# Kernel optimization log

Hardware: AMD Instinct MI355X
Metric: run time of the kernel (lower is better)

## Reference

```python
import jax, jax.numpy as jnp
import numpy as np

H = 16      # query heads
KV = 4      # kv heads
HD = 128    # head dim
THETA = 10000.0
NEG = -1e9


def _rope_tables(S, dtype):
    inv_freq = 1.0 / (THETA ** (jnp.arange(0, HD, 2, dtype=jnp.float32) / HD))
    ang = jnp.arange(S, dtype=jnp.float32)[:, None] * inv_freq[None, :]  # [S, HD/2]
    emb = jnp.concatenate([ang, ang], axis=-1)  # [S, HD]
    return jnp.cos(emb).astype(dtype), jnp.sin(emb).astype(dtype)


def _rotate_half(x):
    x1, x2 = jnp.split(x, 2, axis=-1)
    return jnp.concatenate([-x2, x1], axis=-1)


def _apply_rope(t, cos, sin):
    # t: [B, h, S, HD]; cos/sin: [S, HD]
    return t * cos[None, None] + _rotate_half(t) * sin[None, None]


def setup_inputs() -> dict:
    key = jax.random.key(0)
    ks = jax.random.split(key, 5)
    B, S, D = 2, 2048, 2048
    sc = 0.02
    return {
        "x": jax.random.normal(ks[0], (B, S, D), jnp.float32),
        "wq": jax.random.normal(ks[1], (D, D), jnp.float32) * sc,
        "wk": jax.random.normal(ks[2], (KV * HD, D), jnp.float32) * sc,
        "wv": jax.random.normal(ks[3], (KV * HD, D), jnp.float32) * sc,
        "wo": jax.random.normal(ks[4], (D, D), jnp.float32) * sc,
    }


def reference(x, wq, wk, wv, wo):
    B, S, D = x.shape
    q = (x @ wq.T).reshape(B, S, H, HD).transpose(0, 2, 1, 3)   # [B,H,S,HD]
    k = (x @ wk.T).reshape(B, S, KV, HD).transpose(0, 2, 1, 3)  # [B,KV,S,HD]
    v = (x @ wv.T).reshape(B, S, KV, HD).transpose(0, 2, 1, 3)

    cos, sin = _rope_tables(S, x.dtype)
    q = _apply_rope(q, cos, sin)
    k = _apply_rope(k, cos, sin)

    # GQA: repeat kv heads to match query heads (q_group_num = H // KV)
    k = jnp.repeat(k, H // KV, axis=1)  # [B,H,S,HD]
    v = jnp.repeat(v, H // KV, axis=1)

    scores = jnp.einsum("bhqd,bhkd->bhqk", q, k) / jnp.sqrt(jnp.float32(HD)).astype(x.dtype)
    causal = jnp.where(jnp.tril(jnp.ones((S, S), bool)), 0.0, NEG).astype(jnp.float32)
    attn = jax.nn.softmax(scores.astype(jnp.float32) + causal, axis=-1).astype(x.dtype)

    out = jnp.einsum("bhqk,bhkd->bhqd", attn, v)  # [B,H,S,HD]
    out = out.transpose(0, 2, 1, 3).reshape(B, S, D)
    return out @ wo.T
```

## Files before the change

### kernel.cpp

```cpp
#include <hip/hip_runtime.h>
#include <math.h>

typedef unsigned short u16;
typedef __attribute__((ext_vector_type(8))) short short8;
typedef __attribute__((ext_vector_type(8))) __bf16 bf16x8;
typedef __attribute__((ext_vector_type(4))) float floatx4;
typedef __attribute__((ext_vector_type(16))) float floatx16;
typedef __attribute__((ext_vector_type(4))) unsigned short u16x4;
typedef __attribute__((ext_vector_type(4))) float float4v;
typedef __attribute__((ext_vector_type(4))) unsigned int uint4v;

static __device__ __forceinline__ float b2f(u16 u) {
  unsigned int x = ((unsigned int)u) << 16;
  return __builtin_bit_cast(float, x);
}
static __device__ __forceinline__ u16 f2b(float f) {
  unsigned int x = __builtin_bit_cast(unsigned int, f);
  x += 0x7fffu + ((x >> 16) & 1u);
  return (u16)(x >> 16);
}
static __device__ __forceinline__ unsigned int pk2(float lo, float hi) {
  unsigned int r;
  asm("v_cvt_pk_bf16_f32 %0, %1, %2" : "=v"(r) : "v"(lo), "v"(hi));
  return r;
}
static __device__ __forceinline__ void gload_lds16(const void* g, void* l) {
  __builtin_amdgcn_global_load_lds(
      (const __attribute__((address_space(1))) unsigned int*)g,
      (__attribute__((address_space(3))) unsigned int*)l, 16, 0, 0);
}

__global__ __launch_bounds__(256) void cvt5_kernel(
    const float* __restrict__ x, const float* __restrict__ wq,
    const float* __restrict__ wk, const float* __restrict__ wv,
    const float* __restrict__ wo, u16* __restrict__ xb, u16* __restrict__ wqb,
    u16* __restrict__ wkb, u16* __restrict__ wvb, u16* __restrict__ wob) {
  int bid = blockIdx.x;
  const float* in;
  u16* out;
  int i0;
  if (bid < 8192) { in = x; out = xb; i0 = bid; }
  else if (bid < 12288) { in = wq; out = wqb; i0 = bid - 8192; }
  else if (bid < 13312) { in = wk; out = wkb; i0 = bid - 12288; }
  else if (bid < 14336) { in = wv; out = wvb; i0 = bid - 13312; }
  else { in = wo; out = wob; i0 = bid - 14336; }
  int i = i0 * 256 + threadIdx.x;
  float4v v = reinterpret_cast<const float4v*>(in)[i];
  u16x4 o;
  o[0] = f2b(v[0]); o[1] = f2b(v[1]); o[2] = f2b(v[2]); o[3] = f2b(v[3]);
  reinterpret_cast<u16x4*>(out)[i] = o;
}

__global__ __launch_bounds__(256) void rope_table_kernel(float* __restrict__ ct,
                                                         float* __restrict__ st) {
  int idx = blockIdx.x * 256 + threadIdx.x;
  int s = idx >> 6, j = idx & 63;
  float inv = powf(10000.0f, -(float)j * (1.0f / 64.0f));
  float ang = (float)s * inv;
  ct[idx] = cosf(ang);
  st[idx] = sinf(ang);
}

__global__ __launch_bounds__(256) void rope_k_kernel(const u16* __restrict__ in,
                                                     u16* __restrict__ out,
                                                     const float* __restrict__ ct,
                                                     const float* __restrict__ st) {
  int idx = blockIdx.x * 256 + threadIdx.x;
  int jc = idx & 7;
  int rest = idx >> 3;
  int h = rest & 3;
  int bs = rest >> 2;
  int s = bs & 2047;
  int b = bs >> 11;
  int j0 = jc * 8;
  size_t inoff = (size_t)bs * 3072 + 2048 + h * 128 + j0;
  short8 lo = *reinterpret_cast<const short8*>(&in[inoff]);
  short8 hi = *reinterpret_cast<const short8*>(&in[inoff + 64]);
  short8 o0, o1;
#pragma unroll
  for (int e = 0; e < 8; ++e) {
    float c = ct[s * 64 + j0 + e], sn = st[s * 64 + j0 + e];
    float t1 = b2f((u16)lo[e]);
    float t2 = b2f((u16)hi[e]);
    o0[e] = (short)f2b(t1 * c - t2 * sn);
    o1[e] = (short)f2b(t2 * c + t1 * sn);
  }
  size_t ooff = ((size_t)(b * 4 + h) * 2048 + s) * 128 + j0;
  *reinterpret_cast<short8*>(&out[ooff]) = o0;
  *reinterpret_cast<short8*>(&out[ooff + 64]) = o1;
}

__global__ __launch_bounds__(256) void vtrans_kernel(const u16* __restrict__ in,
                                                     u16* __restrict__ out) {
  __shared__ u16 t[128][66];
  int s0 = blockIdx.x * 64;
  int b = blockIdx.y >> 2, kv = blockIdx.y & 3;
  int tid = threadIdx.x;
#pragma unroll
  for (int it = 0; it < 32; ++it) {
    int idx = it * 256 + tid;
    int sl = idx >> 7, d = idx & 127;
    t[d][sl] = in[(size_t)(b * 2048 + s0 + sl) * 3072 + 2560 + kv * 128 + d];
  }
  __syncthreads();
#pragma unroll
  for (int it = 0; it < 32; ++it) {
    int idx = it * 256 + tid;
    int d = idx >> 6, sl = idx & 63;
    out[(size_t)((b * 4 + kv) * 128 + d) * 2048 + s0 + sl] = t[d][sl];
  }
}

static __device__ __forceinline__ void store_out(u16* p, float v) { *p = f2b(v); }
static __device__ __forceinline__ void store_out(float* p, float v) { *p = v; }

template <typename OutT>
__global__ __launch_bounds__(256) void gemm_bt(const u16* __restrict__ A,
                                               const u16* __restrict__ B,
                                               OutT* __restrict__ C, int M, int N, int K) {
  __shared__ __align__(16) u16 Al[128 * 32];
  __shared__ __align__(16) u16 Bl[128 * 32];
  const int tid = threadIdx.x;
  const int lane = tid & 63;
  const int w = tid >> 6;
  const int wr = w >> 1, wc = w & 1;
  const int lr = lane & 15, lg = lane >> 4;
  const int brow = blockIdx.y, bcol = blockIdx.x;
  const int r0 = lane >> 2, kp = lane & 3;
  const u16* Ag = A + (size_t)(brow * 128) * K;
  const u16* Bg = B + (size_t)(bcol * 128) * K;
  floatx4 acc[4][4] = {};
  for (int k0 = 0; k0 < K; k0 += 32) {
#pragma unroll
    for (int j = 0; j < 2; ++j) {
      int c = w * 2 + j;
      int row = c * 16 + r0;
      gload_lds16(Ag + (size_t)row * K + k0 + kp * 8, &Al[c * 512]);
      gload_lds16(Bg + (size_t)row * K + k0 + kp * 8, &Bl[c * 512]);
    }
    __syncthreads();
    bf16x8 af[4], bfr[4];
#pragma unroll
    for (int m = 0; m < 4; ++m)
      af[m] = *reinterpret_cast<const bf16x8*>(&Al[(wr * 64 + m * 16 + lr) * 32 + lg * 8]);
#pragma unroll
    for (int n = 0; n < 4; ++n)
      bfr[n] = *reinterpret_cast<const bf16x8*>(&Bl[(wc * 64 + n * 16 + lr) * 32 + lg * 8]);
#pragma unroll
    for (int m = 0; m < 4; ++m)
#pragma unroll
      for (int n = 0; n < 4; ++n)
        acc[m][n] = __builtin_amdgcn_mfma_f32_16x16x32_bf16(af[m], bfr[n], acc[m][n], 0, 0, 0);
    __syncthreads();
  }
#pragma unroll
  for (int m = 0; m < 4; ++m) {
    int row = brow * 128 + wr * 64 + m * 16 + lg * 4;
#pragma unroll
    for (int n = 0; n < 4; ++n) {
      int col = bcol * 128 + wc * 64 + n * 16 + lr;
#pragma unroll
      for (int i = 0; i < 4; ++i) store_out(&C[(size_t)(row + i) * N + col], acc[m][n][i]);
    }
  }
}

__global__ __launch_bounds__(256, 2) void attn_kernel(const u16* __restrict__ QKV,
                                                      const u16* __restrict__ K,
                                                      const u16* __restrict__ V,
                                                      const float* __restrict__ ct,
                                                      const float* __restrict__ st,
                                                      u16* __restrict__ O) {
  __shared__ __align__(16) u16 Kl[2][64 * 128];
  __shared__ __align__(16) u16 Vl[2][128 * 64];
  const int tid = threadIdx.x, lane = tid & 63, w = tid >> 6;
  const int ql = lane & 31, h2 = lane >> 5;
  const int bx = blockIdx.x;
  const int tt = bx >> 5;
  const int t = (bx < 256) ? (15 - tt) : (tt - 8);
  const int bh = bx & 31;
  const int b = bh >> 4, hh = bh & 15, kv = hh >> 2;
  const u16* Kp = K + (size_t)(b * 4 + kv) * 2048 * 128;
  const u16* Vp = V + (size_t)(b * 4 + kv) * 128 * 2048;
  const int q0w = t * 128 + w * 32;
  const int qg = q0w + ql;

  bf16x8 qa[8];
  {
    const u16* qp = QKV + ((size_t)(b * 2048 + qg)) * 3072 + hh * 128;
    short8 rr[8];
#pragma unroll
    for (int dk = 0; dk < 8; ++dk)
      rr[dk] = *reinterpret_cast<const short8*>(qp + dk * 16 + h2 * 8);
    const float* cb = ct + (size_t)qg * 64;
    const float* sb = st + (size_t)qg * 64;
#pragma unroll
    for (int dk = 0; dk < 4; ++dk) {
      short8 olo, ohi;
#pragma unroll
      for (int e = 0; e < 8; ++e) {
        int j = dk * 16 + h2 * 8 + e;
        float c = cb[j], sn = sb[j];
        float t1 = b2f((u16)rr[dk][e]);
        float t2 = b2f((u16)rr[dk + 4][e]);
        olo[e] = (short)f2b(t1 * c - t2 * sn);
        ohi[e] = (short)f2b(t2 * c + t1 * sn);
      }
      qa[dk] = __builtin_bit_cast(bf16x8, olo);
      qa[dk + 4] = __builtin_bit_cast(bf16x8, ohi);
    }
  }

  float m_r = -1e30f, l_r = 0.0f;
  floatx16 oacc[4] = {};

  auto stage = [&](int buf, int kb) {
#pragma unroll
    for (int j = 0; j < 4; ++j) {
      int slot = j * 256 + tid;
      int row = slot >> 4, d16 = slot & 15;
      gload_lds16(Kp + (size_t)(kb * 64 + row) * 128 + (d16 ^ (row & 15)) * 8,
                  &Kl[buf][(j * 256 + w * 64) * 8]);
      int d = slot >> 3, k8 = slot & 7;
      gload_lds16(Vp + (size_t)d * 2048 + kb * 64 + (k8 ^ (d & 7)) * 8,
                  &Vl[buf][(j * 256 + w * 64) * 8]);
    }
  };

  stage(0, 0);
  __syncthreads();
  const int nkb = 2 * t + 2;
  const float cl = 0.08838834764831845f * 1.44269504088896f;
  int cur = 0;
  for (int kb = 0; kb < nkb; ++kb) {
    if (kb + 1 < nkb) stage(cur ^ 1, kb + 1);
    if (kb * 64 <= q0w + 31) {
      const u16* Klc = Kl[cur];
      const u16* Vlc = Vl[cur];
      floatx16 sT0 = {}, sT1 = {};
      __builtin_amdgcn_s_setprio(1);
#pragma unroll
      for (int dk = 0; dk < 8; ++dk) {
        int row0 = ql, row1 = 32 + ql;
        bf16x8 ak0 = *reinterpret_cast<const bf16x8*>(
            &Klc[row0 * 128 + (((dk * 2 + h2) ^ (row0 & 15))) * 8]);
        bf16x8 ak1 = *reinterpret_cast<const bf16x8*>(
            &Klc[row1 * 128 + (((dk * 2 + h2) ^ (row1 & 15))) * 8]);
        sT0 = __builtin_amdgcn_mfma_f32_32x32x16_bf16(ak0, qa[dk], sT0, 0, 0, 0);
        sT1 = __builtin_amdgcn_mfma_f32_32x32x16_bf16(ak1, qa[dk], sT1, 0, 0, 0);
      }
      __builtin_amdgcn_s_setprio(0);
      float x[32];
      const bool domask = (kb * 64 + 63 > q0w);
#pragma unroll
      for (int rg = 0; rg < 16; ++rg) {
        int kloc0 = (rg & 3) + 8 * (rg >> 2) + 4 * h2;
        float v0 = sT0[rg] * cl;
        float v1 = sT1[rg] * cl;
        if (domask) {
          if (kb * 64 + kloc0 > qg) v0 = -1e30f;
          if (kb * 64 + 32 + kloc0 > qg) v1 = -1e30f;
        }
        x[rg] = v0;
        x[16 + rg] = v1;
      }
      float mx[16];
#pragma unroll
      for (int i = 0; i < 16; ++i) mx[i] = fmaxf(x[i], x[i + 16]);
#pragma unroll
      for (int i = 0; i < 8; ++i) mx[i] = fmaxf(mx[i], mx[i + 8]);
#pragma unroll
      for (int i = 0; i < 4; ++i) mx[i] = fmaxf(mx[i], mx[i + 4]);
      float tmax = fmaxf(fmaxf(mx[0], mx[1]), fmaxf(mx[2], mx[3]));
      tmax = fmaxf(tmax, __shfl_xor(tmax, 32));
      if (!__all(tmax - m_r <= 11.0f)) {
        float mn = fmaxf(m_r, tmax);
        float al = exp2f(m_r - mn);
        m_r = mn;
        l_r *= al;
#pragma unroll
        for (int rg = 0; rg < 16; ++rg) {
          int rowq = (rg & 3) + 8 * (rg >> 2) + 4 * h2;
          float arow = __shfl(al, rowq);
          oacc[0][rg] *= arow; oacc[1][rg] *= arow;
          oacc[2][rg] *= arow; oacc[3][rg] *= arow;
        }
      }
      float p[32];
#pragma unroll
      for (int i = 0; i < 32; ++i) p[i] = exp2f(x[i] - m_r);
      float sm[16];
#pragma unroll
      for (int i = 0; i < 16; ++i) sm[i] = p[i] + p[i + 16];
#pragma unroll
      for (int i = 0; i < 8; ++i) sm[i] += sm[i + 8];
#pragma unroll
      for (int i = 0; i < 4; ++i) sm[i] += sm[i + 4];
      float ts = (sm[0] + sm[1]) + (sm[2] + sm[3]);
      ts += __shfl_xor(ts, 32);
      l_r += ts;
      bf16x8 pa[4];
#pragma unroll
      for (int ka = 0; ka < 2; ++ka) {
        const int o = ka * 16;
        unsigned int x0 = pk2(p[o + 0], p[o + 1]);
        unsigned int x1 = pk2(p[o + 2], p[o + 3]);
        unsigned int y0 = pk2(p[o + 4], p[o + 5]);
        unsigned int y1 = pk2(p[o + 6], p[o + 7]);
        asm volatile("v_permlane32_swap_b32 %0, %1" : "+v"(x0), "+v"(y0));
        asm volatile("v_permlane32_swap_b32 %0, %1" : "+v"(x1), "+v"(y1));
        uint4v f0 = {x0, x1, y0, y1};
        pa[ka * 2] = __builtin_bit_cast(bf16x8, f0);
        unsigned int z0 = pk2(p[o + 8], p[o + 9]);
        unsigned int z1 = pk2(p[o + 10], p[o + 11]);
        unsigned int u0 = pk2(p[o + 12], p[o + 13]);
        unsigned int u1 = pk2(p[o + 14], p[o + 15]);
        asm volatile("v_permlane32_swap_b32 %0, %1" : "+v"(z0), "+v"(u0));
        asm volatile("v_permlane32_swap_b32 %0, %1" : "+v"(z1), "+v"(u1));
        uint4v f1 = {z0, z1, u0, u1};
        pa[ka * 2 + 1] = __builtin_bit_cast(bf16x8, f1);
      }
      __builtin_amdgcn_s_setprio(1);
#pragma unroll
      for (int tb = 0; tb < 4; ++tb) {
        int d = tb * 32 + ql;
#pragma unroll
        for (int ks = 0; ks < 4; ++ks) {
          bf16x8 bv = *reinterpret_cast<const bf16x8*>(
              &Vlc[d * 64 + (((ks * 2 + h2) ^ (d & 7))) * 8]);
          oacc[tb] = __builtin_amdgcn_mfma_f32_32x32x16_bf16(pa[ks], bv, oacc[tb], 0, 0, 0);
        }
      }
      __builtin_amdgcn_s_setprio(0);
    }
    __syncthreads();
    cur ^= 1;
  }
  float linv = 1.0f / l_r;
#pragma unroll
  for (int rg = 0; rg < 16; ++rg) {
    int rowq = (rg & 3) + 8 * (rg >> 2) + 4 * h2;
    float inv = __shfl(linv, rowq);
    int qrow = t * 128 + w * 32 + rowq;
    size_t base = ((size_t)(b * 2048 + qrow)) * 2048 + hh * 128 + ql;
#pragma unroll
    for (int tb = 0; tb < 4; ++tb)
      O[base + tb * 32] = f2b(oacc[tb][rg] * inv);
  }
}

extern "C" void kernel_launch(void* const* d_in, const int* in_sizes, int n_in,
                              void* d_out, int out_size, void* d_ws, size_t ws_size,
                              hipStream_t stream) {
  const float* x  = (const float*)d_in[0];
  const float* wq = (const float*)d_in[1];
  const float* wk = (const float*)d_in[2];
  const float* wv = (const float*)d_in[3];
  const float* wo = (const float*)d_in[4];
  float* out = (float*)d_out;
  char* ws = (char*)d_ws;
  size_t off = 0;
  auto alloc = [&](size_t bytes) -> void* {
    void* p = ws + off;
    off = (off + bytes + 255) & ~(size_t)255;
    return p;
  };
  u16* xb   = (u16*)alloc(4096ull * 2048 * 2);
  u16* wqb  = (u16*)alloc(2048ull * 2048 * 2);
  u16* wkb  = (u16*)alloc(512ull * 2048 * 2);
  u16* wvb  = (u16*)alloc(512ull * 2048 * 2);
  u16* wob  = (u16*)alloc(2048ull * 2048 * 2);
  u16* qkv  = (u16*)alloc(4096ull * 3072 * 2);
  u16* kr   = (u16*)alloc(4096ull * 512 * 2);
  u16* vtb  = (u16*)alloc(4096ull * 512 * 2);
  float* ctab = (float*)alloc(2048ull * 64 * 4);
  float* stab = (float*)alloc(2048ull * 64 * 4);
  u16* attnb = xb;
  (void)in_sizes; (void)n_in; (void)out_size; (void)ws_size;

  cvt5_kernel<<<18432, 256, 0, stream>>>(x, wq, wk, wv, wo, xb, wqb, wkb, wvb, wob);
  rope_table_kernel<<<512, 256, 0, stream>>>(ctab, stab);

  gemm_bt<u16><<<dim3(24, 32), 256, 0, stream>>>(xb, wqb, qkv, 4096, 3072, 2048);

  rope_k_kernel<<<512, 256, 0, stream>>>(qkv, kr, ctab, stab);
  vtrans_kernel<<<dim3(32, 8), 256, 0, stream>>>(qkv, vtb);

  attn_kernel<<<dim3(512), 256, 0, stream>>>(qkv, kr, vtb, ctab, stab, attnb);

  gemm_bt<float><<<dim3(16, 32), 256, 0, stream>>>(attnb, wob, out, 4096, 2048, 2048);
}
```

Measured before the change: 245.3 us.

## Split long causal attention tiles across blocks and merge partials in a combine kernel

The attention kernel now balances work per block. Each long query tile (t=8..15) has its KV range split at block 17: the first half of the grid handles the prefix, and the second half handles the remainder plus one short tile. Partial outputs are written in bf16 together with their row max and row sum, and a new combine kernel merges the two halves with a log-sum-exp rescale. This aims to equalise per-block work under the causal triangle, at the cost of an extra kernel launch, partial-buffer traffic, and bf16 rounding of the unnormalised partial outputs.

```diff
diff --git a/kernel.cpp b/kernel.cpp
--- a/kernel.cpp
+++ b/kernel.cpp
@@ -165,54 +165,23 @@
   }
 }
 
-__global__ __launch_bounds__(256, 2) void attn_kernel(const u16* __restrict__ QKV,
-                                                      const u16* __restrict__ K,
-                                                      const u16* __restrict__ V,
-                                                      const float* __restrict__ ct,
-                                                      const float* __restrict__ st,
-                                                      u16* __restrict__ O) {
+__global__ __launch_bounds__(256, 2) void attn_kernel(
+    const u16* __restrict__ QKV, const u16* __restrict__ K,
+    const u16* __restrict__ V, const float* __restrict__ ct,
+    const float* __restrict__ st, u16* __restrict__ O, u16* __restrict__ Opart,
+    float* __restrict__ Mpart, float* __restrict__ Lpart) {
   __shared__ __align__(16) u16 Kl[2][64 * 128];
   __shared__ __align__(16) u16 Vl[2][128 * 64];
   const int tid = threadIdx.x, lane = tid & 63, w = tid >> 6;
   const int ql = lane & 31, h2 = lane >> 5;
-  const int bx = blockIdx.x;
-  const int tt = bx >> 5;
-  const int t = (bx < 256) ? (15 - tt) : (tt - 8);
-  const int bh = bx & 31;
+  const int idx = blockIdx.x;
+  const int bh = idx & 31, pp = (idx >> 5) & 7, half = idx >> 8;
   const int b = bh >> 4, hh = bh & 15, kv = hh >> 2;
+  const int t_l = 15 - pp, t_s = pp;
+  const int pidx = bh * 8 + pp;
   const u16* Kp = K + (size_t)(b * 4 + kv) * 2048 * 128;
   const u16* Vp = V + (size_t)(b * 4 + kv) * 128 * 2048;
-  const int q0w = t * 128 + w * 32;
-  const int qg = q0w + ql;
-
-  bf16x8 qa[8];
-  {
-    const u16* qp = QKV + ((size_t)(b * 2048 + qg)) * 3072 + hh * 128;
-    short8 rr[8];
-#pragma unroll
-    for (int dk = 0; dk < 8; ++dk)
-      rr[dk] = *reinterpret_cast<const short8*>(qp + dk * 16 + h2 * 8);
-    const float* cb = ct + (size_t)qg * 64;
-    const float* sb = st + (size_t)qg * 64;
-#pragma unroll
-    for (int dk = 0; dk < 4; ++dk) {
-      short8 olo, ohi;
-#pragma unroll
-      for (int e = 0; e < 8; ++e) {
-        int j = dk * 16 + h2 * 8 + e;
-        float c = cb[j], sn = sb[j];
-        float t1 = b2f((u16)rr[dk][e]);
-        float t2 = b2f((u16)rr[dk + 4][e]);
-        olo[e] = (short)f2b(t1 * c - t2 * sn);
-        ohi[e] = (short)f2b(t2 * c + t1 * sn);
-      }
-      qa[dk] = __builtin_bit_cast(bf16x8, olo);
-      qa[dk + 4] = __builtin_bit_cast(bf16x8, ohi);
-    }
-  }
-
-  float m_r = -1e30f, l_r = 0.0f;
-  floatx16 oacc[4] = {};
+  const float cl = 0.08838834764831845f * 1.44269504088896f;
 
   auto stage = [&](int buf, int kb) {
 #pragma unroll
@@ -227,125 +196,206 @@
     }
   };
 
-  stage(0, 0);
-  __syncthreads();
-  const int nkb = 2 * t + 2;
-  const float cl = 0.08838834764831845f * 1.44269504088896f;
-  int cur = 0;
-  for (int kb = 0; kb < nkb; ++kb) {
-    if (kb + 1 < nkb) stage(cur ^ 1, kb + 1);
-    if (kb * 64 <= q0w + 31) {
-      const u16* Klc = Kl[cur];
-      const u16* Vlc = Vl[cur];
-      floatx16 sT0 = {}, sT1 = {};
-      __builtin_amdgcn_s_setprio(1);
-#pragma unroll
-      for (int dk = 0; dk < 8; ++dk) {
-        int row0 = ql, row1 = 32 + ql;
-        bf16x8 ak0 = *reinterpret_cast<const bf16x8*>(
-            &Klc[row0 * 128 + (((dk * 2 + h2) ^ (row0 & 15))) * 8]);
-        bf16x8 ak1 = *reinterpret_cast<const bf16x8*>(
-            &Klc[row1 * 128 + (((dk * 2 + h2) ^ (row1 & 15))) * 8]);
-        sT0 = __builtin_amdgcn_mfma_f32_32x32x16_bf16(ak0, qa[dk], sT0, 0, 0, 0);
-        sT1 = __builtin_amdgcn_mfma_f32_32x32x16_bf16(ak1, qa[dk], sT1, 0, 0, 0);
+  auto run_segment = [&](int t, int kvs, int kve, int part) {
+    const int q0w = t * 128 + w * 32;
+    const int qg = q0w + ql;
+    bf16x8 qa[8];
+    {
+      const u16* qp = QKV + ((size_t)(b * 2048 + qg)) * 3072 + hh * 128;
+      short8 rr[8];
+#pragma unroll
+      for (int dk = 0; dk < 8; ++dk)
+        rr[dk] = *reinterpret_cast<const short8*>(qp + dk * 16 + h2 * 8);
+      const float* cb = ct + (size_t)qg * 64;
+      const float* sb = st + (size_t)qg * 64;
+#pragma unroll
+      for (int dk = 0; dk < 4; ++dk) {
+        short8 olo, ohi;
+#pragma unroll
+        for (int e = 0; e < 8; ++e) {
+          int j = dk * 16 + h2 * 8 + e;
+          float c = cb[j], sn = sb[j];
+          float t1 = b2f((u16)rr[dk][e]);
+          float t2 = b2f((u16)rr[dk + 4][e]);
+          olo[e] = (short)f2b(t1 * c - t2 * sn);
+          ohi[e] = (short)f2b(t2 * c + t1 * sn);
+        }
+        qa[dk] = __builtin_bit_cast(bf16x8, olo);
+        qa[dk + 4] = __builtin_bit_cast(bf16x8, ohi);
       }
-      __builtin_amdgcn_s_setprio(0);
-      float x[32];
-      const bool domask = (kb * 64 + 63 > q0w);
+    }
+    float m_r = -1e30f, l_r = 0.0f;
+    floatx16 oacc[4] = {};
+    stage(0, kvs);
+    __syncthreads();
+    int cur = 0;
+    for (int kb = kvs; kb < kve; ++kb) {
+      if (kb + 1 < kve) stage(cur ^ 1, kb + 1);
+      if (kb * 64 <= q0w + 31) {
+        const u16* Klc = Kl[cur];
+        const u16* Vlc = Vl[cur];
+        floatx16 sT0 = {}, sT1 = {};
+        __builtin_amdgcn_s_setprio(1);
+#pragma unroll
+        for (int dk = 0; dk < 8; ++dk) {
+          int row0 = ql, row1 = 32 + ql;
+          bf16x8 ak0 = *reinterpret_cast<const bf16x8*>(
+              &Klc[row0 * 128 + (((dk * 2 + h2) ^ (row0 & 15))) * 8]);
+          bf16x8 ak1 = *reinterpret_cast<const bf16x8*>(
+              &Klc[row1 * 128 + (((dk * 2 + h2) ^ (row1 & 15))) * 8]);
+          sT0 = __builtin_amdgcn_mfma_f32_32x32x16_bf16(ak0, qa[dk], sT0, 0, 0, 0);
+          sT1 = __builtin_amdgcn_mfma_f32_32x32x16_bf16(ak1, qa[dk], sT1, 0, 0, 0);
+        }
+        __builtin_amdgcn_s_setprio(0);
+        float x[32];
+        const bool domask = (kb * 64 + 63 > q0w);
+#pragma unroll
+        for (int rg = 0; rg < 16; ++rg) {
+          int kloc0 = (rg & 3) + 8 * (rg >> 2) + 4 * h2;
+          float v0 = sT0[rg] * cl;
+          float v1 = sT1[rg] * cl;
+          if (domask) {
+            if (kb * 64 + kloc0 > qg) v0 = -1e30f;
+            if (kb * 64 + 32 + kloc0 > qg) v1 = -1e30f;
+          }
+          x[rg] = v0;
+          x[16 + rg] = v1;
+        }
+        float mx[16];
+#pragma unroll
+        for (int i = 0; i < 16; ++i) mx[i] = fmaxf(x[i], x[i + 16]);
+#pragma unroll
+        for (int i = 0; i < 8; ++i) mx[i] = fmaxf(mx[i], mx[i + 8]);
+#pragma unroll
+        for (int i = 0; i < 4; ++i) mx[i] = fmaxf(mx[i], mx[i + 4]);
+        float tmax = fmaxf(fmaxf(mx[0], mx[1]), fmaxf(mx[2], mx[3]));
+        tmax = fmaxf(tmax, __shfl_xor(tmax, 32));
+        if (!__all(tmax - m_r <= 11.0f)) {
+          float mn = fmaxf(m_r, tmax);
+          float al = exp2f(m_r - mn);
+          m_r = mn;
+          l_r *= al;
+#pragma unroll
+          for (int rg = 0; rg < 16; ++rg) {
+            int rowq = (rg & 3) + 8 * (rg >> 2) + 4 * h2;
+            float arow = __shfl(al, rowq);
+            oacc[0][rg] *= arow; oacc[1][rg] *= arow;
+            oacc[2][rg] *= arow; oacc[3][rg] *= arow;
+          }
+        }
+        float p[32];
+#pragma unroll
+        for (int i = 0; i < 32; ++i) p[i] = exp2f(x[i] - m_r);
+        float sm[16];
+#pragma unroll
+        for (int i = 0; i < 16; ++i) sm[i] = p[i] + p[i + 16];
+#pragma unroll
+        for (int i = 0; i < 8; ++i) sm[i] += sm[i + 8];
+#pragma unroll
+        for (int i = 0; i < 4; ++i) sm[i] += sm[i + 4];
+        float ts = (sm[0] + sm[1]) + (sm[2] + sm[3]);
+        ts += __shfl_xor(ts, 32);
+        l_r += ts;
+        bf16x8 pa[4];
+#pragma unroll
+        for (int ka = 0; ka < 2; ++ka) {
+          const int o = ka * 16;
+          unsigned int x0 = pk2(p[o + 0], p[o + 1]);
+          unsigned int x1 = pk2(p[o + 2], p[o + 3]);
+          unsigned int y0 = pk2(p[o + 4], p[o + 5]);
+          unsigned int y1 = pk2(p[o + 6], p[o + 7]);
+          asm volatile("v_permlane32_swap_b32 %0, %1" : "+v"(x0), "+v"(y0));
+          asm volatile("v_permlane32_swap_b32 %0, %1" : "+v"(x1), "+v"(y1));
+          uint4v f0 = {x0, x1, y0, y1};
+          pa[ka * 2] = __builtin_bit_cast(bf16x8, f0);
+          unsigned int z0 = pk2(p[o + 8], p[o + 9]);
+          unsigned int z1 = pk2(p[o + 10], p[o + 11]);
+          unsigned int u0 = pk2(p[o + 12], p[o + 13]);
+          unsigned int u1 = pk2(p[o + 14], p[o + 15]);
+          asm volatile("v_permlane32_swap_b32 %0, %1" : "+v"(z0), "+v"(u0));
+          asm volatile("v_permlane32_swap_b32 %0, %1" : "+v"(z1), "+v"(u1));
+          uint4v f1 = {z0, z1, u0, u1};
+          pa[ka * 2 + 1] = __builtin_bit_cast(bf16x8, f1);
+        }
+        __builtin_amdgcn_s_setprio(1);
+#pragma unroll
+        for (int tb = 0; tb < 4; ++tb) {
+          int d = tb * 32 + ql;
+#pragma unroll
+          for (int ks = 0; ks < 4; ++ks) {
+            bf16x8 bv = *reinterpret_cast<const bf16x8*>(
+                &Vlc[d * 64 + (((ks * 2 + h2) ^ (d & 7))) * 8]);
+            oacc[tb] = __builtin_amdgcn_mfma_f32_32x32x16_bf16(pa[ks], bv, oacc[tb], 0, 0, 0);
+          }
+        }
+        __builtin_amdgcn_s_setprio(0);
+      }
+      __syncthreads();
+      cur ^= 1;
+    }
+    if (part < 0) {
+      float linv = 1.0f / l_r;
 #pragma unroll
       for (int rg = 0; rg < 16; ++rg) {
-        int kloc0 = (rg & 3) + 8 * (rg >> 2) + 4 * h2;
-        float v0 = sT0[rg] * cl;
-        float v1 = sT1[rg] * cl;
-        if (domask) {
-          if (kb * 64 + kloc0 > qg) v0 = -1e30f;
-          if (kb * 64 + 32 + kloc0 > qg) v1 = -1e30f;
-        }
-        x[rg] = v0;
-        x[16 + rg] = v1;
+        int rowq = (rg & 3) + 8 * (rg >> 2) + 4 * h2;
+        float inv = __shfl(linv, rowq);
+        int qrow = t * 128 + w * 32 + rowq;
+        size_t base = ((size_t)(b * 2048 + qrow)) * 2048 + hh * 128 + ql;
+#pragma unroll
+        for (int tb = 0; tb < 4; ++tb)
+          O[base + tb * 32] = f2b(oacc[tb][rg] * inv);
       }
-      float mx[16];
-#pragma unroll
-      for (int i = 0; i < 16; ++i) mx[i] = fmaxf(x[i], x[i + 16]);
-#pragma unroll
-      for (int i = 0; i < 8; ++i) mx[i] = fmaxf(mx[i], mx[i + 8]);
-#pragma unroll
-      for (int i = 0; i < 4; ++i) mx[i] = fmaxf(mx[i], mx[i + 4]);
-      float tmax = fmaxf(fmaxf(mx[0], mx[1]), fmaxf(mx[2], mx[3]));
-      tmax = fmaxf(tmax, __shfl_xor(tmax, 32));
-      if (!__all(tmax - m_r <= 11.0f)) {
-        float mn = fmaxf(m_r, tmax);
-        float al = exp2f(m_r - mn);
-        m_r = mn;
-        l_r *= al;
-#pragma unroll
-        for (int rg = 0; rg < 16; ++rg) {
-          int rowq = (rg & 3) + 8 * (rg >> 2) + 4 * h2;
-          float arow = __shfl(al, rowq);
-          oacc[0][rg] *= arow; oacc[1][rg] *= arow;
-          oacc[2][rg] *= arow; oacc[3][rg] *= arow;
-        }
+    } else {
+      size_t pb = ((size_t)(part * 256 + pidx)) * 128;
+#pragma unroll
+      for (int rg = 0; rg < 16; ++rg) {
+        int rowq = (rg & 3) + 8 * (rg >> 2) + 4 * h2;
+        size_t base = (pb + w * 32 + rowq) * 128 + ql;
+#pragma unroll
+        for (int tb = 0; tb < 4; ++tb)
+          Opart[base + tb * 32] = f2b(oacc[tb][rg]);
       }
-      float p[32];
-#pragma unroll
-      for (int i = 0; i < 32; ++i) p[i] = exp2f(x[i] - m_r);
-      float sm[16];
-#pragma unroll
-      for (int i = 0; i < 16; ++i) sm[i] = p[i] + p[i + 16];
-#pragma unroll
-      for (int i = 0; i < 8; ++i) sm[i] += sm[i + 8];
-#pragma unroll
-      for (int i = 0; i < 4; ++i) sm[i] += sm[i + 4];
-      float ts = (sm[0] + sm[1]) + (sm[2] + sm[3]);
-      ts += __shfl_xor(ts, 32);
-      l_r += ts;
-      bf16x8 pa[4];
-#pragma unroll
-      for (int ka = 0; ka < 2; ++ka) {
-        const int o = ka * 16;
-        unsigned int x0 = pk2(p[o + 0], p[o + 1]);
-        unsigned int x1 = pk2(p[o + 2], p[o + 3]);
-        unsigned int y0 = pk2(p[o + 4], p[o + 5]);
-        unsigned int y1 = pk2(p[o + 6], p[o + 7]);
-        asm volatile("v_permlane32_swap_b32 %0, %1" : "+v"(x0), "+v"(y0));
-        asm volatile("v_permlane32_swap_b32 %0, %1" : "+v"(x1), "+v"(y1));
-        uint4v f0 = {x0, x1, y0, y1};
-        pa[ka * 2] = __builtin_bit_cast(bf16x8, f0);
-        unsigned int z0 = pk2(p[o + 8], p[o + 9]);
-        unsigned int z1 = pk2(p[o + 10], p[o + 11]);
-        unsigned int u0 = pk2(p[o + 12], p[o + 13]);
-        unsigned int u1 = pk2(p[o + 14], p[o + 15]);
-        asm volatile("v_permlane32_swap_b32 %0, %1" : "+v"(z0), "+v"(u0));
-        asm volatile("v_permlane32_swap_b32 %0, %1" : "+v"(z1), "+v"(u1));
-        uint4v f1 = {z0, z1, u0, u1};
-        pa[ka * 2 + 1] = __builtin_bit_cast(bf16x8, f1);
+      if (h2 == 0) {
+        Mpart[pb + w * 32 + ql] = m_r;
+        Lpart[pb + w * 32 + ql] = l_r;
       }
-      __builtin_amdgcn_s_setprio(1);
-#pragma unroll
-      for (int tb = 0; tb < 4; ++tb) {
-        int d = tb * 32 + ql;
-#pragma unroll
-        for (int ks = 0; ks < 4; ++ks) {
-          bf16x8 bv = *reinterpret_cast<const bf16x8*>(
-              &Vlc[d * 64 + (((ks * 2 + h2) ^ (d & 7))) * 8]);
-          oacc[tb] = __builtin_amdgcn_mfma_f32_32x32x16_bf16(pa[ks], bv, oacc[tb], 0, 0, 0);
-        }
-      }
-      __builtin_amdgcn_s_setprio(0);
-    }
-    __syncthreads();
-    cur ^= 1;
-  }
-  float linv = 1.0f / l_r;
-#pragma unroll
-  for (int rg = 0; rg < 16; ++rg) {
-    int rowq = (rg & 3) + 8 * (rg >> 2) + 4 * h2;
-    float inv = __shfl(linv, rowq);
-    int qrow = t * 128 + w * 32 + rowq;
-    size_t base = ((size_t)(b * 2048 + qrow)) * 2048 + hh * 128 + ql;
-#pragma unroll
-    for (int tb = 0; tb < 4; ++tb)
-      O[base + tb * 32] = f2b(oacc[tb][rg] * inv);
+    }
+  };
+
+  if (half == 0) {
+    run_segment(t_l, 0, 17, 0);
+  } else {
+    run_segment(t_l, 17, 2 * t_l + 2, 1);
+    run_segment(t_s, 0, 2 * t_s + 2, -1);
+  }
+}
+
+__global__ __launch_bounds__(256) void combine_kernel(
+    const u16* __restrict__ Opart, const float* __restrict__ Mpart,
+    const float* __restrict__ Lpart, u16* __restrict__ O) {
+  int pidx = blockIdx.x;
+  int bh = pidx >> 3, pp = pidx & 7;
+  int b = bh >> 4, hh = bh & 15;
+  int t_l = 15 - pp;
+  int tid = threadIdx.x;
+  int row = tid >> 1, colbase = (tid & 1) * 64;
+  size_t pb0 = (size_t)pidx * 128 + row;
+  size_t pb1 = (size_t)(256 + pidx) * 128 + row;
+  float m0 = Mpart[pb0], m1 = Mpart[pb1];
+  float l0 = Lpart[pb0], l1 = Lpart[pb1];
+  float M = fmaxf(m0, m1);
+  float w0 = exp2f(m0 - M), w1 = exp2f(m1 - M);
+  float inv = 1.0f / (w0 * l0 + w1 * l1);
+  size_t ob = ((size_t)(b * 2048 + t_l * 128 + row)) * 2048 + hh * 128 + colbase;
+#pragma unroll
+  for (int k = 0; k < 8; ++k) {
+    short8 o0 = *reinterpret_cast<const short8*>(&Opart[pb0 * 128 + colbase + k * 8]);
+    short8 o1 = *reinterpret_cast<const short8*>(&Opart[pb1 * 128 + colbase + k * 8]);
+    short8 r;
+#pragma unroll
+    for (int e = 0; e < 8; ++e)
+      r[e] = (short)f2b((w0 * b2f((u16)o0[e]) + w1 * b2f((u16)o1[e])) * inv);
+    *reinterpret_cast<short8*>(&O[ob + k * 8]) = r;
   }
 }
 
@@ -375,6 +425,9 @@
   u16* vtb  = (u16*)alloc(4096ull * 512 * 2);
   float* ctab = (float*)alloc(2048ull * 64 * 4);
   float* stab = (float*)alloc(2048ull * 64 * 4);
+  u16* opart  = (u16*)alloc(2ull * 256 * 128 * 128 * 2);
+  float* mpart = (float*)alloc(2ull * 256 * 128 * 4);
+  float* lpart = (float*)alloc(2ull * 256 * 128 * 4);
   u16* attnb = xb;
   (void)in_sizes; (void)n_in; (void)out_size; (void)ws_size;
 
@@ -386,7 +439,9 @@
   rope_k_kernel<<<512, 256, 0, stream>>>(qkv, kr, ctab, stab);
   vtrans_kernel<<<dim3(32, 8), 256, 0, stream>>>(qkv, vtb);
 
-  attn_kernel<<<dim3(512), 256, 0, stream>>>(qkv, kr, vtb, ctab, stab, attnb);
+  attn_kernel<<<dim3(512), 256, 0, stream>>>(qkv, kr, vtb, ctab, stab, attnb,
+                                             opart, mpart, lpart);
+  combine_kernel<<<dim3(256), 256, 0, stream>>>(opart, mpart, lpart, attnb);
 
   gemm_bt<float><<<dim3(16, 32), 256, 0, stream>>>(attnb, wob, out, 4096, 2048, 2048);
 }
```

Result: faster. 235.8 us (-3.9%).
